# Kernel tuning notes

Hardware: AMD Instinct MI355X
Metric: run time of the kernel (lower is better)

Reference implementation:

```python
import jax, jax.numpy as jnp
import numpy as np

N_QUBITS = 10
N_LAYERS = 6
BATCH = 16384
DIM = 2 ** N_QUBITS


def _apply_1q(state, U, q):
    # state: (B, 2**n) complex64; U: (2,2) complex; wire 0 is most significant (PennyLane convention)
    B = state.shape[0]
    L = 2 ** q
    R = 2 ** (N_QUBITS - q - 1)
    st = state.reshape(B, L, 2, R)
    st = jnp.einsum('xy,blyr->blxr', U, st)
    return st.reshape(B, DIM)


def _apply_cnot(state, c, t):
    # CNOT with control wire c, target wire t
    B = state.shape[0]
    st = state.reshape((B,) + (2,) * N_QUBITS)
    s0 = jnp.take(st, 0, axis=c + 1)
    s1 = jnp.take(st, 1, axis=c + 1)
    t_ax = t + 1 if t < c else t  # target axis index after control axis removed
    s1 = jnp.flip(s1, axis=t_ax)  # Pauli-X on target for control=1 branch
    st = jnp.stack([s0, s1], axis=c + 1)
    return st.reshape(B, DIM)


def _rot(phi, theta, omega):
    # PennyLane Rot(phi, theta, omega) = RZ(omega) RY(theta) RZ(phi)
    c = jnp.cos(0.5 * theta)
    s = jnp.sin(0.5 * theta)
    u00 = jnp.exp(-0.5j * (phi + omega)) * c
    u01 = -jnp.exp(0.5j * (phi - omega)) * s
    u10 = jnp.exp(-0.5j * (phi - omega)) * s
    u11 = jnp.exp(0.5j * (phi + omega)) * c
    return jnp.stack([jnp.stack([u00, u01]), jnp.stack([u10, u11])]).astype(jnp.complex64)


def _circuit(x, weights):
    # x: (B, n_qubits) angles; weights: (n_layers, n_qubits, 3)
    B = x.shape[0]
    half = 0.5 * x
    c = jnp.cos(half).astype(jnp.complex64)
    s = jnp.sin(half).astype(jnp.complex64)
    # AngleEmbedding (default rotation='X'): RX(x_i)|0> = [cos(x/2), -i sin(x/2)]
    qvec = jnp.stack([c, -1j * s], axis=-1)  # (B, n, 2)
    state = qvec[:, 0]
    for q in range(1, N_QUBITS):  # product state via successive Kronecker products
        state = (state[:, :, None] * qvec[:, q][:, None, :]).reshape(B, -1)
    # StronglyEntanglingLayers: per layer, Rot on every wire then ring of CNOTs with range r
    for l in range(N_LAYERS):
        for w in range(N_QUBITS):
            U = _rot(weights[l, w, 0], weights[l, w, 1], weights[l, w, 2])
            state = _apply_1q(state, U, w)
        r = (l % (N_QUBITS - 1)) + 1  # default ranges
        for w in range(N_QUBITS):
            state = _apply_cnot(state, w, (w + r) % N_QUBITS)
    probs = state.real ** 2 + state.imag ** 2  # (B, 2**n)
    bits = (jnp.arange(DIM)[:, None] >> (N_QUBITS - 1 - jnp.arange(N_QUBITS))) & 1
    signs = (1 - 2 * bits).astype(probs.dtype)  # (2**n, n): PauliZ eigenvalues per qubit
    return probs @ signs  # (B, n_qubits) expvals


def setup_inputs() -> dict:
    key = jax.random.key(0)
    k1, k2, k3, k4 = jax.random.split(key, 4)
    x = jax.random.normal(k1, (BATCH, N_QUBITS), dtype=jnp.float32)
    q_layers = jax.random.normal(k2, (N_LAYERS, N_QUBITS, 3), dtype=jnp.float32)
    fc_w = jax.random.normal(k3, (1, N_QUBITS), dtype=jnp.float32) / np.sqrt(N_QUBITS)
    fc_b = jax.random.normal(k4, (1,), dtype=jnp.float32) * 0.01
    return {"x": x, "q_layers": q_layers, "fc_w": fc_w, "fc_b": fc_b}


def reference(x, q_layers, fc_w, fc_b):
    z = _circuit(x, q_layers)  # (B, n_qubits)
    return z @ fc_w.T + fc_b   # (B, 1)
```

## Files before the change

### kernel.cpp

```cpp
#include <hip/hip_runtime.h>
#include <math.h>

#define NQ 10
#define DIM 1024
#define NLAYERS 6
#define BATCH 16384

typedef float v2f __attribute__((ext_vector_type(2)));

struct F2Mat { unsigned short row[NQ]; };

constexpr F2Mat f2_id() {
    F2Mat m{}; for (int i = 0; i < NQ; ++i) m.row[i] = (unsigned short)(1u << i);
    return m;
}
constexpr F2Mat f2_mul(F2Mat A, F2Mat B) {
    F2Mat C{};
    for (int i = 0; i < NQ; ++i) {
        unsigned r = 0;
        for (int j = 0; j < NQ; ++j) if ((A.row[i] >> j) & 1u) r ^= B.row[j];
        C.row[i] = (unsigned short)r;
    }
    return C;
}
constexpr F2Mat L_mat(int pc, int pt) {
    F2Mat m = f2_id();
    m.row[pt] = (unsigned short)((1u << pt) | (1u << pc));
    return m;
}
constexpr F2Mat ring_K(int l) {
    int r = l % (NQ - 1) + 1;
    F2Mat K = f2_id();
    for (int w = 0; w < NQ; ++w) K = f2_mul(K, L_mat(NQ - 1 - w, NQ - 1 - (w + r) % NQ));
    return K;
}
constexpr F2Mat ring_Kinv(int l) {
    int r = l % (NQ - 1) + 1;
    F2Mat K = f2_id();
    for (int w = NQ - 1; w >= 0; --w) K = f2_mul(K, L_mat(NQ - 1 - w, NQ - 1 - (w + r) % NQ));
    return K;
}
constexpr unsigned kapply(F2Mat K, unsigned j) {
    unsigned r = 0;
    for (int i = 0; i < NQ; ++i) r |= (unsigned)(__builtin_popcount(K.row[i] & j) & 1) << i;
    return r;
}

struct Mix { unsigned mk[4]; };
constexpr unsigned mix_apply(Mix m, unsigned h) {
    unsigned r = 0;
    for (int b = 0; b < 4; ++b) if ((h >> b) & 1) r ^= m.mk[b];
    return r;
}
constexpr int rank_of(const unsigned (&v)[6]) {
    unsigned a[6] = {v[0], v[1], v[2], v[3], v[4], v[5]};
    int rank = 0;
    for (int bit = 5; bit >= 0; --bit) {
        int piv = -1;
        for (int i = rank; i < 6; ++i) if ((a[i] >> bit) & 1) { piv = i; break; }
        if (piv < 0) continue;
        unsigned t = a[piv]; a[piv] = a[rank]; a[rank] = t;
        for (int i = 0; i < 6; ++i) if (i != rank && ((a[i] >> bit) & 1)) a[i] ^= a[rank];
        ++rank;
    }
    return rank;
}
constexpr int read_rank(F2Mat K, Mix m) {
    unsigned img[6] = {};
    for (int b = 0; b < 6; ++b) {
        unsigned t = kapply(K, 1u << b);
        img[b] = (t ^ mix_apply(m, t >> 6)) & 63u;
    }
    return rank_of(img);
}
constexpr Mix mix_candidate(int a) {
    Mix m{{0, 0, 0, 0}};
    if (a == 0) return m;
    if (a <= 6) {
        for (int i = 0; i < 4; ++i) m.mk[i] = 1u << ((i + (a - 1)) % 6);
        return m;
    }
    for (int i = 0; i < 4; ++i)
        m.mk[i] = (1u << ((i + (a - 7)) % 6)) | (1u << ((i + (a - 7) + 3) % 6));
    return m;
}
constexpr Mix find_mix(F2Mat K) {
    Mix best{{0, 0, 0, 0}};
    int bestr = read_rank(K, best);
    for (int a = 1; a < 13 && bestr < 6; ++a) {
        Mix c = mix_candidate(a);
        int r = read_rank(K, c);
        if (r > bestr) { best = c; bestr = r; }
    }
    return best;
}
struct RelayTabs { unsigned wb[16]; unsigned rb[16]; unsigned ck[6]; };
constexpr RelayTabs make_relay(int l) {
    F2Mat K = ring_K(l);
    Mix mx = find_mix(K);
    RelayTabs t{};
    for (int v = 0; v < 16; ++v) {
        t.wb[v] = ((unsigned)v << 6) ^ mix_apply(mx, (unsigned)v);
        unsigned kv = kapply(K, (unsigned)v << 6);
        t.rb[v] = kv ^ mix_apply(mx, kv >> 6);
    }
    for (int b = 0; b < 6; ++b) {
        unsigned kb = kapply(K, 1u << b);
        t.ck[b] = kb ^ mix_apply(mx, kb >> 6);
    }
    return t;
}

struct DevTabs { unsigned short K[NLAYERS - 1][NQ]; unsigned short K5i[NQ]; };
constexpr DevTabs make_devtabs() {
    DevTabs d{};
    for (int l = 0; l < NLAYERS - 1; ++l) {
        F2Mat K = ring_K(l);
        for (int i = 0; i < NQ; ++i) d.K[l][i] = K.row[i];
    }
    F2Mat K5 = ring_Kinv(NLAYERS - 1);
    for (int i = 0; i < NQ; ++i) d.K5i[i] = K5.row[i];
    return d;
}
__constant__ DevTabs dKT = make_devtabs();
__device__ __forceinline__ unsigned kap_rt(const unsigned short* rows, unsigned j) {
    unsigned r = 0;
#pragma unroll
    for (int i = 0; i < NQ; ++i) r |= (unsigned)(__popc((unsigned)rows[i] & j) & 1) << i;
    return r;
}

#define WS_CS   0
#define WS_DIAG 128
#define WS_W    12416

__global__ __launch_bounds__(256) void prep_kernel(const float* __restrict__ qw,
                                                   const float* __restrict__ fcw,
                                                   float* __restrict__ ws) {
    const int part = blockIdx.x >> 2;
    const int j = (blockIdx.x & 3) * 256 + threadIdx.x;
    float2* D = (float2*)(ws + WS_DIAG);
    if (part == 0) {
        if (j < NLAYERS * NQ) {
            float s, c;
            sincosf(0.5f * qw[3 * j + 1], &s, &c);
            ws[WS_CS + 2 * j]     = c;
            ws[WS_CS + 2 * j + 1] = s;
        }
        {
            unsigned jj = kap_rt(dKT.K5i, (unsigned)j);
            float w = 0.f;
#pragma unroll
            for (int k = 0; k < NQ; ++k)
                w += fcw[k] * (float)(1 - 2 * (int)((jj >> (NQ - 1 - k)) & 1u));
            ws[WS_W + j] = w;
        }
        {
            float ang = 0.f;
#pragma unroll
            for (int q = 0; q < NQ; ++q)
                ang += qw[3 * q + 0] * (float)(1 - 2 * (int)((j >> (NQ - 1 - q)) & 1));
            float sn, cn; sincosf(-0.5f * ang, &sn, &cn);
            D[j] = make_float2(cn, sn);
        }
    } else {
        const int l = part - 1;
        unsigned kj = kap_rt(dKT.K[l], (unsigned)j);
        float ang = 0.f;
#pragma unroll
        for (int q = 0; q < NQ; ++q) {
            ang += qw[3 * ((l + 1) * NQ + q) + 0] * (float)(1 - 2 * (int)(((unsigned)j >> (NQ - 1 - q)) & 1u));
            ang += qw[3 * (l * NQ + q) + 2]       * (float)(1 - 2 * (int)((kj >> (NQ - 1 - q)) & 1u));
        }
        float sn, cn; sincosf(-0.5f * ang, &sn, &cn);
        D[(l + 1) * DIM + j] = make_float2(cn, sn);
    }
}

template<int P>
__device__ __forceinline__ void gate_reg(v2f st[2][16], float c, float s) {
    constexpr int vm = 1 << (P - 6);
#pragma unroll
    for (int v = 0; v < 16; ++v) {
        if (v & vm) continue;
#pragma unroll
        for (int e = 0; e < 2; ++e) {
            v2f a = st[e][v], b = st[e][v | vm];
            st[e][v]      = c * a - s * b;
            st[e][v | vm] = s * a + c * b;
        }
    }
}

template<int CTRL>
__device__ __forceinline__ float dpp_x(float x) {
    return __int_as_float(__builtin_amdgcn_update_dpp(__float_as_int(x), __float_as_int(x),
                                                      CTRL, 0xF, 0xF, true));
}
template<int MASK>
__device__ __forceinline__ float lane_xor(float x) {
    if constexpr (MASK == 1)      return dpp_x<0xB1>(x);
    else if constexpr (MASK == 2) return dpp_x<0x4E>(x);
    else if constexpr (MASK == 4) return __int_as_float(__builtin_amdgcn_ds_swizzle(__float_as_int(x), 0x101F));
    else if constexpr (MASK == 8) return __int_as_float(__builtin_amdgcn_ds_swizzle(__float_as_int(x), 0x201F));
    else                          return __int_as_float(__builtin_amdgcn_ds_swizzle(__float_as_int(x), 0x401F));
}
template<int MASK>
__device__ __forceinline__ void gate_lane(v2f st[2][16], int lane, float c, float s) {
    const float co = (lane & MASK) ? s : -s;
#pragma unroll
    for (int v = 0; v < 16; ++v)
#pragma unroll
        for (int e = 0; e < 2; ++e) {
            v2f a = st[e][v];
            v2f o;
            o.x = lane_xor<MASK>(a.x);
            o.y = lane_xor<MASK>(a.y);
            st[e][v] = c * a + co * o;
        }
}

__device__ __forceinline__ float bperm32(float x, int addr) {
    return __int_as_float(__builtin_amdgcn_ds_bpermute(addr, __float_as_int(x)));
}
__device__ __forceinline__ void gate_mask32(v2f st[2][16], int lane, float c, float s) {
    const float co = (lane & 32) ? s : -s;
    const int addr = (lane ^ 32) << 2;
#pragma unroll
    for (int v = 0; v < 16; ++v)
#pragma unroll
        for (int e = 0; e < 2; ++e) {
            v2f a = st[e][v];
            v2f o;
            o.x = bperm32(a.x, addr);
            o.y = bperm32(a.y, addr);
            st[e][v] = c * a + co * o;
        }
}

template<int L>
__device__ __forceinline__ void relayout(v2f st[2][16], int lane, v2f* buf) {
    constexpr RelayTabs RT = make_relay(L);
    unsigned rl = 0;
#pragma unroll
    for (int b = 0; b < 6; ++b) rl ^= ((lane >> b) & 1) ? RT.ck[b] : 0u;
#pragma unroll
    for (int e = 0; e < 2; ++e) {
#pragma unroll
        for (int v = 0; v < 16; ++v) buf[RT.wb[v] ^ (unsigned)lane] = st[e][v];
        asm volatile("s_waitcnt lgkmcnt(0)" ::: "memory");
#pragma unroll
        for (int v = 0; v < 16; ++v) st[e][v] = buf[RT.rb[v] ^ rl];
    }
}

__device__ __forceinline__ void apply_diag(v2f st[2][16], const v2f* __restrict__ g,
                                           int lane) {
#pragma unroll
    for (int v = 0; v < 16; ++v) {
        v2f G = g[(v << 6) | lane];
        v2f nG; nG.x = -G.y; nG.y = G.x;
#pragma unroll
        for (int e = 0; e < 2; ++e) {
            v2f a = st[e][v];
            st[e][v] = a.xx * G + a.yy * nG;
        }
    }
}

template<int L>
__device__ __forceinline__ void do_layer(v2f st[2][16], int lane,
                                         const float* __restrict__ ws, v2f* buf) {
    const float* cs = ws + WS_CS + 2 * (L * NQ);
    gate_reg<9>(st, cs[0], cs[1]);
    gate_reg<8>(st, cs[2], cs[3]);
    gate_reg<7>(st, cs[4], cs[5]);
    gate_reg<6>(st, cs[6], cs[7]);
    gate_mask32(st, lane, cs[8], cs[9]);
    gate_lane<16>(st, lane, cs[10], cs[11]);
    gate_lane<8>(st, lane, cs[12], cs[13]);
    gate_lane<4>(st, lane, cs[14], cs[15]);
    gate_lane<2>(st, lane, cs[16], cs[17]);
    gate_lane<1>(st, lane, cs[18], cs[19]);
    if constexpr (L < NLAYERS - 1) {
        relayout<L>(st, lane, buf);
        apply_diag(st, (const v2f*)(ws + WS_DIAG) + (L + 1) * DIM, lane);
    }
}

__global__ __launch_bounds__(256, 4) void qsim_kernel(const float* __restrict__ x,
                                                      const float* __restrict__ ws,
                                                      const float* __restrict__ fcb,
                                                      float* __restrict__ out) {
    __shared__ v2f lbuf[4][DIM];
    const int lane = threadIdx.x & 63;
    const int wid  = threadIdx.x >> 6;
    const int b0   = blockIdx.x * 8 + wid * 2;
    v2f* buf = lbuf[wid];

    v2f st[2][16];
#pragma unroll
    for (int e = 0; e < 2; ++e) {
        float cq[NQ], sq[NQ];
#pragma unroll
        for (int q = 0; q < NQ; ++q) {
            float ss, cc;
            __sincosf(0.5f * x[(b0 + e) * NQ + q], &ss, &cc);
            sq[q] = ss; cq[q] = cc;
        }
#pragma unroll
        for (int v = 0; v < 16; ++v) {
            const int i = (v << 6) | lane;
            float mag = 1.f;
#pragma unroll
            for (int q = 0; q < NQ; ++q) {
                int bit = (i >> (NQ - 1 - q)) & 1;
                mag *= bit ? sq[q] : cq[q];
            }
            const int k = __popc(i) & 3;
            float re = (k == 0) ? mag : ((k == 2) ? -mag : 0.f);
            float im = (k == 1) ? -mag : ((k == 3) ? mag : 0.f);
            v2f a; a.x = re; a.y = im;
            st[e][v] = a;
        }
    }

    apply_diag(st, (const v2f*)(ws + WS_DIAG), lane);
    do_layer<0>(st, lane, ws, buf);
    do_layer<1>(st, lane, ws, buf);
    do_layer<2>(st, lane, ws, buf);
    do_layer<3>(st, lane, ws, buf);
    do_layer<4>(st, lane, ws, buf);
    do_layer<5>(st, lane, ws, buf);

    const float* W = ws + WS_W;
    float acc0 = 0.f, acc1 = 0.f;
#pragma unroll
    for (int v = 0; v < 16; ++v) {
        float w = W[(v << 6) | lane];
        float p0 = st[0][v].x * st[0][v].x + st[0][v].y * st[0][v].y;
        float p1 = st[1][v].x * st[1][v].x + st[1][v].y * st[1][v].y;
        acc0 = fmaf(p0, w, acc0);
        acc1 = fmaf(p1, w, acc1);
    }
#pragma unroll
    for (int off = 32; off > 0; off >>= 1) {
        acc0 += __shfl_down(acc0, off, 64);
        acc1 += __shfl_down(acc1, off, 64);
    }
    if (lane == 0) {
        float bias = fcb[0];
        out[b0]     = acc0 + bias;
        out[b0 + 1] = acc1 + bias;
    }
}

extern "C" void kernel_launch(void* const* d_in, const int* in_sizes, int n_in,
                              void* d_out, int out_size, void* d_ws, size_t ws_size,
                              hipStream_t stream) {
    const float* x   = (const float*)d_in[0];
    const float* qw  = (const float*)d_in[1];
    const float* fcw = (const float*)d_in[2];
    const float* fcb = (const float*)d_in[3];
    float* out = (float*)d_out;
    float* ws  = (float*)d_ws;

    prep_kernel<<<24, 256, 0, stream>>>(qw, fcw, ws);
    qsim_kernel<<<BATCH / 8, 256, 0, stream>>>(x, ws, fcb, out);
}
```

Measured before the change: 184.0 us.

## Replace cross-lane gates on high lane bits with an LDS relayout swap

Four gates per layer that mixed amplitudes across lanes via ds_bpermute and ds_swizzle are replaced. An extra LDS relayout now swaps lane bits 2-5 with register bits 6-9, so those gates run as in-register butterflies. The per-layer relayout tables are composed with this swap, and the final weight table accounts for the changed bit order. This trades 4 gates' worth of cross-lane shuffles (two per amplitude per gate) for one more full LDS write/read round trip per layer. That adds LDS traffic, a wait and added index bookkeeping.

Measured after the change: 183.5 us. About the same (-0.3%).

```diff
diff --git a/kernel.cpp b/kernel.cpp
--- a/kernel.cpp
+++ b/kernel.cpp
@@ -44,6 +44,19 @@
     unsigned r = 0;
     for (int i = 0; i < NQ; ++i) r |= (unsigned)(__builtin_popcount(K.row[i] & j) & 1) << i;
     return r;
+}
+
+constexpr int s_bit(int i) { return (i >= 2 && i <= 5) ? i + 4 : (i >= 6 && i <= 9) ? i - 4 : i; }
+constexpr F2Mat S_mat() {
+    F2Mat m{};
+    for (int i = 0; i < NQ; ++i) m.row[i] = (unsigned short)(1u << s_bit(i));
+    return m;
+}
+constexpr F2Mat SK_mat(int l) {
+    F2Mat K = ring_K(l);
+    F2Mat m{};
+    for (int i = 0; i < NQ; ++i) m.row[i] = K.row[s_bit(i)];
+    return m;
 }
 
 struct Mix { unsigned mk[4]; };
@@ -65,10 +78,10 @@
     }
     return rank;
 }
-constexpr int read_rank(F2Mat K, Mix m) {
+constexpr int read_rank(F2Mat M, Mix m) {
     unsigned img[6] = {};
     for (int b = 0; b < 6; ++b) {
-        unsigned t = kapply(K, 1u << b);
+        unsigned t = kapply(M, 1u << b);
         img[b] = (t ^ mix_apply(m, t >> 6)) & 63u;
     }
     return rank_of(img);
@@ -84,31 +97,34 @@
         m.mk[i] = (1u << ((i + (a - 7)) % 6)) | (1u << ((i + (a - 7) + 3) % 6));
     return m;
 }
-constexpr Mix find_mix(F2Mat K) {
+constexpr Mix find_mix(F2Mat M) {
     Mix best{{0, 0, 0, 0}};
-    int bestr = read_rank(K, best);
+    int bestr = read_rank(M, best);
     for (int a = 1; a < 13 && bestr < 6; ++a) {
         Mix c = mix_candidate(a);
-        int r = read_rank(K, c);
+        int r = read_rank(M, c);
         if (r > bestr) { best = c; bestr = r; }
     }
     return best;
 }
 struct RelayTabs { unsigned wb[16]; unsigned rb[16]; unsigned ck[6]; };
-constexpr RelayTabs make_relay(int l) {
-    F2Mat K = ring_K(l);
-    Mix mx = find_mix(K);
+constexpr RelayTabs make_relay_m(F2Mat M) {
+    Mix mx = find_mix(M);
     RelayTabs t{};
     for (int v = 0; v < 16; ++v) {
         t.wb[v] = ((unsigned)v << 6) ^ mix_apply(mx, (unsigned)v);
-        unsigned kv = kapply(K, (unsigned)v << 6);
+        unsigned kv = kapply(M, (unsigned)v << 6);
         t.rb[v] = kv ^ mix_apply(mx, kv >> 6);
     }
     for (int b = 0; b < 6; ++b) {
-        unsigned kb = kapply(K, 1u << b);
+        unsigned kb = kapply(M, 1u << b);
         t.ck[b] = kb ^ mix_apply(mx, kb >> 6);
     }
     return t;
+}
+constexpr RelayTabs relay_for(int sel) {
+    if (sel == 0) return make_relay_m(S_mat());
+    return make_relay_m(SK_mat(sel - 1));
 }
 
 struct DevTabs { unsigned short K[NLAYERS - 1][NQ]; unsigned short K5i[NQ]; };
@@ -128,6 +144,9 @@
 #pragma unroll
     for (int i = 0; i < NQ; ++i) r |= (unsigned)(__popc((unsigned)rows[i] & j) & 1) << i;
     return r;
+}
+__device__ __forceinline__ unsigned s_swap_rt(unsigned j) {
+    return (j & 3u) | ((j & 0x3Cu) << 4) | ((j >> 4) & 0x3Cu);
 }
 
 #define WS_CS   0
@@ -148,7 +167,7 @@
             ws[WS_CS + 2 * j + 1] = s;
         }
         {
-            unsigned jj = kap_rt(dKT.K5i, (unsigned)j);
+            unsigned jj = kap_rt(dKT.K5i, s_swap_rt((unsigned)j));
             float w = 0.f;
 #pragma unroll
             for (int k = 0; k < NQ; ++k)
@@ -199,11 +218,8 @@
 }
 template<int MASK>
 __device__ __forceinline__ float lane_xor(float x) {
-    if constexpr (MASK == 1)      return dpp_x<0xB1>(x);
-    else if constexpr (MASK == 2) return dpp_x<0x4E>(x);
-    else if constexpr (MASK == 4) return __int_as_float(__builtin_amdgcn_ds_swizzle(__float_as_int(x), 0x101F));
-    else if constexpr (MASK == 8) return __int_as_float(__builtin_amdgcn_ds_swizzle(__float_as_int(x), 0x201F));
-    else                          return __int_as_float(__builtin_amdgcn_ds_swizzle(__float_as_int(x), 0x401F));
+    if constexpr (MASK == 1) return dpp_x<0xB1>(x);
+    else                     return dpp_x<0x4E>(x);
 }
 template<int MASK>
 __device__ __forceinline__ void gate_lane(v2f st[2][16], int lane, float c, float s) {
@@ -220,27 +236,9 @@
         }
 }
 
-__device__ __forceinline__ float bperm32(float x, int addr) {
-    return __int_as_float(__builtin_amdgcn_ds_bpermute(addr, __float_as_int(x)));
-}
-__device__ __forceinline__ void gate_mask32(v2f st[2][16], int lane, float c, float s) {
-    const float co = (lane & 32) ? s : -s;
-    const int addr = (lane ^ 32) << 2;
-#pragma unroll
-    for (int v = 0; v < 16; ++v)
-#pragma unroll
-        for (int e = 0; e < 2; ++e) {
-            v2f a = st[e][v];
-            v2f o;
-            o.x = bperm32(a.x, addr);
-            o.y = bperm32(a.y, addr);
-            st[e][v] = c * a + co * o;
-        }
-}
-
-template<int L>
+template<int SEL>
 __device__ __forceinline__ void relayout(v2f st[2][16], int lane, v2f* buf) {
-    constexpr RelayTabs RT = make_relay(L);
+    constexpr RelayTabs RT = relay_for(SEL);
     unsigned rl = 0;
 #pragma unroll
     for (int b = 0; b < 6; ++b) rl ^= ((lane >> b) & 1) ? RT.ck[b] : 0u;
@@ -276,14 +274,15 @@
     gate_reg<8>(st, cs[2], cs[3]);
     gate_reg<7>(st, cs[4], cs[5]);
     gate_reg<6>(st, cs[6], cs[7]);
-    gate_mask32(st, lane, cs[8], cs[9]);
-    gate_lane<16>(st, lane, cs[10], cs[11]);
-    gate_lane<8>(st, lane, cs[12], cs[13]);
-    gate_lane<4>(st, lane, cs[14], cs[15]);
+    relayout<0>(st, lane, buf);
+    gate_reg<9>(st, cs[8], cs[9]);
+    gate_reg<8>(st, cs[10], cs[11]);
+    gate_reg<7>(st, cs[12], cs[13]);
+    gate_reg<6>(st, cs[14], cs[15]);
     gate_lane<2>(st, lane, cs[16], cs[17]);
     gate_lane<1>(st, lane, cs[18], cs[19]);
     if constexpr (L < NLAYERS - 1) {
-        relayout<L>(st, lane, buf);
+        relayout<L + 1>(st, lane, buf);
         apply_diag(st, (const v2f*)(ws + WS_DIAG) + (L + 1) * DIM, lane);
     }
 }
```
